# Performance work log

Measured on AMD Instinct MI355X. Metric: run time of the kernel, lower is better.

The kernel has to match this reference:

```python
import jax, jax.numpy as jnp
import numpy as np

MODEL_DIM = 1024
BATCH, SEQ = 4, 2048


def setup_inputs() -> dict:
    key = jax.random.key(0)
    kx, kq, kk, kv = jax.random.split(key, 4)
    s = 1.0 / np.sqrt(MODEL_DIM)
    return {
        "x": jax.random.normal(kx, (BATCH, SEQ, MODEL_DIM), dtype=jnp.float32),
        "Wq": jax.random.normal(kq, (MODEL_DIM, MODEL_DIM), dtype=jnp.float32) * s,
        "Wk": jax.random.normal(kk, (MODEL_DIM, MODEL_DIM), dtype=jnp.float32) * s,
        "Wv": jax.random.normal(kv, (MODEL_DIM, MODEL_DIM), dtype=jnp.float32) * s,
    }


def reference(x, Wq, Wk, Wv):
    # nn.Linear(d, d, bias=False): y = x @ W.T ; W stored [out, in]
    q = jnp.einsum("bsd,ed->bse", x, Wq)
    k = jnp.einsum("bsd,ed->bse", x, Wk)
    v = jnp.einsum("bsd,ed->bse", x, Wv)
    scores = jnp.einsum("bqd,bkd->bqk", q, k) / jnp.sqrt(jnp.float32(MODEL_DIM))
    attn = jax.nn.softmax(scores, axis=-1)
    return jnp.einsum("bqk,bkd->bqd", attn, v)
```

## Files before the change

kernel.cpp:

```cpp
#include <hip/hip_runtime.h>
#include <hip/hip_bf16.h>


typedef short bf16x8_t __attribute__((ext_vector_type(8)));
typedef float f32x4_t __attribute__((ext_vector_type(4)));
typedef unsigned short u16x8_t __attribute__((ext_vector_type(8)));

static __device__ __forceinline__ unsigned short f2bf(float f) {
  __hip_bfloat16 h = __float2bfloat16(f);
  return *reinterpret_cast<unsigned short*>(&h);
}

#define GLOAD_LDS16(gp, lp)                                            \
  __builtin_amdgcn_global_load_lds(                                    \
      (const __attribute__((address_space(1))) void*)(gp),             \
      (__attribute__((address_space(3))) void*)(lp), 16, 0, 0)

__global__ __launch_bounds__(256) void cast_all(
    const float* __restrict__ x, const float* __restrict__ Wq,
    const float* __restrict__ Wk, const float* __restrict__ Wv,
    unsigned short* __restrict__ xb, unsigned short* __restrict__ Wqk,
    unsigned short* __restrict__ Wvb, float* __restrict__ rowsum) {
  int i = blockIdx.x * 256 + threadIdx.x;
  const float* src;
  unsigned short* dst;
  int local;
  if (i < 1048576) {
    src = x; dst = xb; local = i;
  } else {
    int j = i - 1048576;
    int seg = j >> 17;
    if (seg >= 3) {
      int l = j - 393216;
      if (l < 1024) {
        float4 zz = {0.f, 0.f, 0.f, 0.f};
        ((float4*)rowsum)[l * 2] = zz;
        ((float4*)rowsum)[l * 2 + 1] = zz;
      }
      return;
    }
    local = j & 131071;
    src = (seg == 0) ? Wq : ((seg == 1) ? Wk : Wv);
    dst = (seg == 0) ? Wqk : ((seg == 1) ? (Wqk + 1048576) : Wvb);
  }
  float4 a = ((const float4*)src)[local * 2];
  float4 b = ((const float4*)src)[local * 2 + 1];
  u16x8_t o;
  o[0] = f2bf(a.x); o[1] = f2bf(a.y); o[2] = f2bf(a.z); o[3] = f2bf(a.w);
  o[4] = f2bf(b.x); o[5] = f2bf(b.y); o[6] = f2bf(b.z); o[7] = f2bf(b.w);
  ((u16x8_t*)dst)[local] = o;
}

template <int EPI, int BN>
__global__ __launch_bounds__(512, 2) void gemm256p(
    const unsigned short* __restrict__ A, const unsigned short* __restrict__ B,
    void* __restrict__ Cv, float* __restrict__ rowsum, int K, int lda,
    int ldb, int ldc, long long sA, long long sB, long long sC, float alpha,
    int rsz) {
  constexpr int NBG = BN / 64;
  constexpr int NH = NBG / 2;
  constexpr int BL = BN / 128;
  constexpr int BNW = BN / 4;
  constexpr int ASZ = 256 * 64;
  constexpr int BSZ = BN * 64;

  __shared__ unsigned short lds[2][ASZ + BSZ];

  const int gx = gridDim.x, gy = gridDim.y;
  const int nwg = gx * gy * gridDim.z;
  const int orig = (blockIdx.z * gy + blockIdx.y) * gx + blockIdx.x;
  const int swz = (orig & 7) * (nwg >> 3) + (orig >> 3);
  const int bx = swz % gx;
  const int tmp = swz / gx;
  const int by = tmp % gy;
  const int z = tmp / gy;

  const int tid = threadIdx.x;
  const int lane = tid & 63;
  const int w = tid >> 6;
  const int wm = w >> 2, wn = w & 3;
  const int m0 = by * 256, n0 = bx * BN;

  A += (long long)z * sA;
  B += (long long)z * sB;

  int sta_row[2][2], sta_col[2][2], sta_lds[2][2];
#pragma unroll
  for (int mh = 0; mh < 2; ++mh)
#pragma unroll
    for (int i = 0; i < 2; ++i) {
      int j = w * 2 + i;
      int l0 = (j >> 3) * 1024 + mh * 512 + (j & 7) * 64;
      int lf = l0 + lane;
      int R = lf >> 3;
      sta_row[mh][i] = R;
      sta_col[mh][i] = ((lf & 7) ^ (R & 7)) * 8;
      sta_lds[mh][i] = l0 * 8;
    }
  int stb_row[2][BL], stb_col[2][BL], stb_lds[2][BL];
#pragma unroll
  for (int nh = 0; nh < 2; ++nh)
#pragma unroll
    for (int i = 0; i < BL; ++i) {
      int l0;
      if (BL == 2) {
        int j = w * 2 + i;
        l0 = (j >> 2) * 512 + nh * 256 + (j & 3) * 64;
      } else {
        int j = w;
        l0 = (j >> 1) * 256 + nh * 128 + (j & 1) * 64;
      }
      int lf = l0 + lane;
      int R = lf >> 3;
      stb_row[nh][i] = R;
      stb_col[nh][i] = ((lf & 7) ^ (R & 7)) * 8;
      stb_lds[nh][i] = ASZ + l0 * 8;
    }

  const int q = lane >> 4, rl = lane & 15;
  int aoff[8][2], boff[NBG][2];
#pragma unroll
  for (int tt = 0; tt < 8; ++tt)
#pragma unroll
    for (int ks = 0; ks < 2; ++ks) {
      int ra = wm * 128 + tt * 16 + rl;
      aoff[tt][ks] = ra * 64 + (((ks * 4 + q) ^ (ra & 7)) * 8);
    }
#pragma unroll
  for (int u = 0; u < NBG; ++u)
#pragma unroll
    for (int ks = 0; ks < 2; ++ks) {
      int rb = wn * BNW + u * 16 + rl;
      boff[u][ks] = ASZ + rb * 64 + (((ks * 4 + q) ^ (rb & 7)) * 8);
    }

  f32x4_t acc[8][NBG];
#pragma unroll
  for (int i = 0; i < 8; ++i)
#pragma unroll
    for (int j = 0; j < NBG; ++j) acc[i][j] = (f32x4_t){0.f, 0.f, 0.f, 0.f};

#define SA(BUFI, MH, K0)                                                    \
  {                                                                         \
    _Pragma("unroll") for (int i_ = 0; i_ < 2; ++i_)                        \
        GLOAD_LDS16(&A[(long long)(m0 + sta_row[MH][i_]) * lda + (K0) +     \
                       sta_col[MH][i_]],                                    \
                    &lds[BUFI][sta_lds[MH][i_]]);                           \
  }
#define SB(BUFI, NH_, K0)                                                   \
  {                                                                         \
    _Pragma("unroll") for (int i_ = 0; i_ < BL; ++i_)                       \
        GLOAD_LDS16(&B[(long long)(n0 + stb_row[NH_][i_]) * ldb + (K0) +    \
                       stb_col[NH_][i_]],                                   \
                    &lds[BUFI][stb_lds[NH_][i_]]);                          \
  }
#define LDAF(MH)                                                            \
  _Pragma("unroll") for (int i_ = 0; i_ < 4; ++i_)                          \
  _Pragma("unroll") for (int ks_ = 0; ks_ < 2; ++ks_)                       \
      af[i_][ks_] = *(const bf16x8_t*)&L[aoff[(MH)*4 + i_][ks_]];
#define LDBG(NH_)                                                           \
  _Pragma("unroll") for (int j_ = 0; j_ < NH; ++j_)                         \
  _Pragma("unroll") for (int ks_ = 0; ks_ < 2; ++ks_)                       \
      bg[j_][ks_] = *(const bf16x8_t*)&L[boff[(NH_)*NH + j_][ks_]];
#define PH_MFMA(MH, NH_)                                                    \
  __builtin_amdgcn_s_barrier();                                             \
  asm volatile("s_waitcnt lgkmcnt(0)" ::: "memory");                        \
  __builtin_amdgcn_sched_barrier(0);                                        \
  __builtin_amdgcn_s_setprio(1);                                            \
  _Pragma("unroll") for (int ks_ = 0; ks_ < 2; ++ks_)                       \
  _Pragma("unroll") for (int i_ = 0; i_ < 4; ++i_)                          \
  _Pragma("unroll") for (int j_ = 0; j_ < NH; ++j_)                         \
      acc[(MH)*4 + i_][(NH_)*NH + j_] =                                     \
          __builtin_amdgcn_mfma_f32_16x16x32_bf16(                          \
              af[i_][ks_], bg[j_][ks_], acc[(MH)*4 + i_][(NH_)*NH + j_],    \
              0, 0, 0);                                                     \
  __builtin_amdgcn_s_setprio(0);                                            \
  __builtin_amdgcn_sched_barrier(0);                                        \
  __builtin_amdgcn_s_barrier();                                             \
  __builtin_amdgcn_sched_barrier(0);

#define VMC_A()                                                             \
  if constexpr (BL == 2) {                                                  \
    asm volatile("s_waitcnt vmcnt(8)" ::: "memory");                        \
  } else {                                                                  \
    asm volatile("s_waitcnt vmcnt(6)" ::: "memory");                        \
  }                                                                         \
  __builtin_amdgcn_sched_barrier(0);
#define VMC_B()                                                             \
  if constexpr (BL == 2) {                                                  \
    asm volatile("s_waitcnt vmcnt(6)" ::: "memory");                        \
  } else {                                                                  \
    asm volatile("s_waitcnt vmcnt(5)" ::: "memory");                        \
  }                                                                         \
  __builtin_amdgcn_sched_barrier(0);
#define VMC_0()                                                             \
  asm volatile("s_waitcnt vmcnt(0)" ::: "memory");                          \
  __builtin_amdgcn_sched_barrier(0);

#define TILE(T, BU, NX)                                                     \
  {                                                                         \
    const unsigned short* L = lds[BU];                                      \
    const int k1 = ((T) + 1) * 64;                                          \
    const int k2 = ((T) + 2) * 64;                                          \
    const bool p1 = ((T) + 1 < NT), p2 = ((T) + 2 < NT);                    \
    bf16x8_t af[4][2], bg[NH][2];                                           \
                                                           \
    LDAF(0);                                                                \
    LDBG(0);                                                                \
    if (p1) SB(NX, 0, k1);                                                  \
    PH_MFMA(0, 0);                                                          \
                                                           \
    LDBG(1);                                                                \
    if (p1) SA(NX, 1, k1);                                                  \
    if (p2) { VMC_A(); } else { VMC_0(); }                                  \
    PH_MFMA(0, 1);                                                          \
                                                           \
    LDAF(1);                                                                \
    if (p2) SA(BU, 0, k2);                                                  \
    PH_MFMA(1, 1);                                                          \
                                                           \
    LDBG(0);                                                                \
    if (p2) { SB(BU, 1, k2); VMC_B(); } else { VMC_0(); }                   \
    PH_MFMA(1, 0);                                                          \
  }

  const int NT = K >> 6;

  SA(0, 0, 0); SB(0, 0, 0); SB(0, 1, 0); SA(0, 1, 0);
  SA(1, 0, 64); SB(1, 1, 64);
  VMC_B();
  __builtin_amdgcn_s_barrier();
  __builtin_amdgcn_sched_barrier(0);

  for (int t = 0; t < NT; t += 2) {
    TILE(t, 0, 1);
    TILE(t + 1, 1, 0);
  }

  if (EPI == 0) {
    unsigned short* C = (unsigned short*)Cv + (long long)z * sC;
#pragma unroll
    for (int tt = 0; tt < 8; ++tt)
#pragma unroll
      for (int u = 0; u < NBG; ++u)
#pragma unroll
        for (int j = 0; j < 4; ++j) {
          int row = m0 + wm * 128 + tt * 16 + q * 4 + j;
          int col = n0 + wn * BNW + u * 16 + rl;
          C[(long long)row * ldc + col] = f2bf(acc[tt][u][j] * alpha);
        }
  } else if (EPI == 1) {
    unsigned short* C = (unsigned short*)Cv + (long long)z * sC;
#pragma unroll
    for (int tt = 0; tt < 8; ++tt)
#pragma unroll
      for (int j = 0; j < 4; ++j) {
        int row = m0 + wm * 128 + tt * 16 + q * 4 + j;
        float sum = 0.f;
#pragma unroll
        for (int u = 0; u < NBG; ++u) {
          float e = __expf(acc[tt][u][j] * alpha);
          int col = n0 + wn * BNW + u * 16 + rl;
          C[(long long)row * ldc + col] = f2bf(e);
          sum += e;
        }
#pragma unroll
        for (int mk = 1; mk <= 8; mk <<= 1) sum += __shfl_xor(sum, mk);
        if (rl == 0) atomicAdd(&rowsum[z * rsz + row], sum);
      }
  } else {
    float* C = (float*)Cv + (long long)z * sC;
#pragma unroll
    for (int tt = 0; tt < 8; ++tt)
#pragma unroll
      for (int j = 0; j < 4; ++j) {
        int row = m0 + wm * 128 + tt * 16 + q * 4 + j;
        float inv = 1.0f / rowsum[z * rsz + row];
#pragma unroll
        for (int u = 0; u < NBG; ++u) {
          int col = n0 + wn * BNW + u * 16 + rl;
          C[(long long)row * ldc + col] = acc[tt][u][j] * inv;
        }
      }
  }
#undef SA
#undef SB
#undef LDAF
#undef LDBG
#undef PH_MFMA
#undef VMC_A
#undef VMC_B
#undef VMC_0
#undef TILE
}

__global__ __launch_bounds__(256) void gemm_nt128(
    const unsigned short* __restrict__ A, const unsigned short* __restrict__ B,
    unsigned short* __restrict__ C, int K, int lda, int ldb, int ldc) {
  __shared__ unsigned short As[128 * 64];
  __shared__ unsigned short Bs[128 * 64];

  const int gx = gridDim.x, gy = gridDim.y;
  const int nwg = gx * gy;
  const int orig = blockIdx.y * gx + blockIdx.x;
  const int swz = (orig & 7) * (nwg >> 3) + (orig >> 3);
  const int bx = swz % gx;
  const int by = swz / gx;

  const int tid = threadIdx.x;
  const int lane = tid & 63;
  const int w = tid >> 6;
  const int wm = w >> 1, wn = w & 1;
  const int m0 = by * 128;
  const int n0 = bx * 128;

  int srow[4], scol[4];
#pragma unroll
  for (int i = 0; i < 4; ++i) {
    int p = w * 256 + i * 64 + lane;
    int r = p >> 3;
    srow[i] = r;
    scol[i] = ((p & 7) ^ (r & 7)) * 8;
  }

  const int q = lane >> 4, rl = lane & 15;
  int aoff[4][2], boff[4][2];
#pragma unroll
  for (int t = 0; t < 4; ++t)
#pragma unroll
    for (int ks = 0; ks < 2; ++ks) {
      int ra = wm * 64 + t * 16 + rl;
      int ca = ks * 4 + q;
      aoff[t][ks] = ra * 64 + ((ca ^ (ra & 7)) * 8);
      int rb = wn * 64 + t * 16 + rl;
      boff[t][ks] = rb * 64 + ((ca ^ (rb & 7)) * 8);
    }

  f32x4_t acc[4][4];
#pragma unroll
  for (int i = 0; i < 4; ++i)
#pragma unroll
    for (int j = 0; j < 4; ++j) acc[i][j] = (f32x4_t){0.f, 0.f, 0.f, 0.f};

  for (int k0 = 0; k0 < K; k0 += 64) {
    __syncthreads();
#pragma unroll
    for (int i = 0; i < 4; ++i) {
      GLOAD_LDS16(&A[(long long)(m0 + srow[i]) * lda + k0 + scol[i]],
                  &As[(w * 4 + i) * 512]);
      GLOAD_LDS16(&B[(long long)(n0 + srow[i]) * ldb + k0 + scol[i]],
                  &Bs[(w * 4 + i) * 512]);
    }
    __syncthreads();

#pragma unroll
    for (int ks = 0; ks < 2; ++ks) {
      bf16x8_t af[4], bgv[4];
#pragma unroll
      for (int t = 0; t < 4; ++t) af[t] = *(const bf16x8_t*)&As[aoff[t][ks]];
#pragma unroll
      for (int u = 0; u < 4; ++u) bgv[u] = *(const bf16x8_t*)&Bs[boff[u][ks]];
#pragma unroll
      for (int i = 0; i < 4; ++i)
#pragma unroll
        for (int j = 0; j < 4; ++j)
          acc[i][j] = __builtin_amdgcn_mfma_f32_16x16x32_bf16(
              af[i], bgv[j], acc[i][j], 0, 0, 0);
    }
  }

#pragma unroll
  for (int t = 0; t < 4; ++t)
#pragma unroll
    for (int u = 0; u < 4; ++u)
#pragma unroll
      for (int j = 0; j < 4; ++j) {
        int row = m0 + wm * 64 + t * 16 + q * 4 + j;
        int col = n0 + wn * 64 + u * 16 + rl;
        C[(long long)row * ldc + col] = f2bf(acc[t][u][j]);
      }
}

extern "C" void kernel_launch(void* const* d_in, const int* in_sizes, int n_in,
                              void* d_out, int out_size, void* d_ws,
                              size_t ws_size, hipStream_t stream) {
  const float* x = (const float*)d_in[0];
  const float* Wq = (const float*)d_in[1];
  const float* Wk = (const float*)d_in[2];
  const float* Wv = (const float*)d_in[3];
  float* out = (float*)d_out;

  unsigned short* xb = (unsigned short*)d_ws;
  unsigned short* Wqk = xb + 8388608;
  unsigned short* Wvb = Wqk + 2097152;
  unsigned short* Cqk = Wvb + 1048576;
  unsigned short* VTb = Cqk + 16777216;
  unsigned short* Scb = VTb + 8388608;
  float* rowsumf = (float*)(Scb + 16777216);

  const dim3 blk(256);
  const dim3 blk512(512);

  cast_all<<<5636, blk, 0, stream>>>(x, Wq, Wk, Wv, xb, Wqk, Wvb, rowsumf);

  gemm256p<0, 256><<<dim3(8, 32, 1), blk512, 0, stream>>>(
      xb, Wqk, Cqk, nullptr, 1024, 1024, 1024, 2048, 0, 0, 0, 1.0f, 0);

  gemm_nt128<<<dim3(64, 8), blk, 0, stream>>>(Wvb, xb, VTb, 1024, 1024, 1024,
                                              8192);

  gemm256p<1, 256><<<dim3(8, 8, 4), blk512, 0, stream>>>(
      Cqk, Cqk + 1024, Scb, rowsumf, 1024, 2048, 2048, 2048,
      (long long)2048 * 2048, (long long)2048 * 2048,
      (long long)2048 * 2048, 0.03125f, 2048);

  gemm256p<2, 128><<<dim3(8, 8, 4), blk512, 0, stream>>>(
      Scb, VTb, out, rowsumf, 2048, 2048, 8192, 1024,
      (long long)2048 * 2048, 2048, (long long)2048 * 1024, 1.0f, 2048);
}
```

Measured before the change: 160.8 us.

## Specialize GEMM to 256x128 tiles with register-prefetched LDS fragments

The templated 256xBN GEMM becomes a single 256x128 kernel. Its per-tile schedule is restructured so the next tile's A and B fragments are read from LDS into registers while the current MFMAs run, with one barrier per phase instead of two and finer vmcnt waits. The QK projection and score GEMMs switch from 256-wide to 128-wide N tiles, doubling their grid size. The intent is to cut LDS-read latency and barrier stalls and to improve CU occupancy, at the cost of more register pressure and less B-tile reuse per workgroup.

```diff
diff --git a/kernel.cpp b/kernel.cpp
--- a/kernel.cpp
+++ b/kernel.cpp
@@ -51,18 +51,14 @@
   ((u16x8_t*)dst)[local] = o;
 }
 
-template <int EPI, int BN>
-__global__ __launch_bounds__(512, 2) void gemm256p(
+template <int EPI>
+__global__ __launch_bounds__(512, 2) void gemmx(
     const unsigned short* __restrict__ A, const unsigned short* __restrict__ B,
     void* __restrict__ Cv, float* __restrict__ rowsum, int K, int lda,
     int ldb, int ldc, long long sA, long long sB, long long sC, float alpha,
     int rsz) {
-  constexpr int NBG = BN / 64;
-  constexpr int NH = NBG / 2;
-  constexpr int BL = BN / 128;
-  constexpr int BNW = BN / 4;
   constexpr int ASZ = 256 * 64;
-  constexpr int BSZ = BN * 64;
+  constexpr int BSZ = 128 * 64;
 
   __shared__ unsigned short lds[2][ASZ + BSZ];
 
@@ -79,7 +75,7 @@
   const int lane = tid & 63;
   const int w = tid >> 6;
   const int wm = w >> 2, wn = w & 3;
-  const int m0 = by * 256, n0 = bx * BN;
+  const int m0 = by * 256, n0 = bx * 128;
 
   A += (long long)z * sA;
   B += (long long)z * sB;
@@ -97,28 +93,19 @@
       sta_col[mh][i] = ((lf & 7) ^ (R & 7)) * 8;
       sta_lds[mh][i] = l0 * 8;
     }
-  int stb_row[2][BL], stb_col[2][BL], stb_lds[2][BL];
-#pragma unroll
-  for (int nh = 0; nh < 2; ++nh)
-#pragma unroll
-    for (int i = 0; i < BL; ++i) {
-      int l0;
-      if (BL == 2) {
-        int j = w * 2 + i;
-        l0 = (j >> 2) * 512 + nh * 256 + (j & 3) * 64;
-      } else {
-        int j = w;
-        l0 = (j >> 1) * 256 + nh * 128 + (j & 1) * 64;
-      }
-      int lf = l0 + lane;
-      int R = lf >> 3;
-      stb_row[nh][i] = R;
-      stb_col[nh][i] = ((lf & 7) ^ (R & 7)) * 8;
-      stb_lds[nh][i] = ASZ + l0 * 8;
-    }
+  int stb_row[2], stb_col[2], stb_lds[2];
+#pragma unroll
+  for (int nh = 0; nh < 2; ++nh) {
+    int l0 = (w >> 1) * 256 + nh * 128 + (w & 1) * 64;
+    int lf = l0 + lane;
+    int R = lf >> 3;
+    stb_row[nh] = R;
+    stb_col[nh] = ((lf & 7) ^ (R & 7)) * 8;
+    stb_lds[nh] = ASZ + l0 * 8;
+  }
 
   const int q = lane >> 4, rl = lane & 15;
-  int aoff[8][2], boff[NBG][2];
+  int aoff[8][2], boff[2][2];
 #pragma unroll
   for (int tt = 0; tt < 8; ++tt)
 #pragma unroll
@@ -127,18 +114,20 @@
       aoff[tt][ks] = ra * 64 + (((ks * 4 + q) ^ (ra & 7)) * 8);
     }
 #pragma unroll
-  for (int u = 0; u < NBG; ++u)
+  for (int u = 0; u < 2; ++u)
 #pragma unroll
     for (int ks = 0; ks < 2; ++ks) {
-      int rb = wn * BNW + u * 16 + rl;
+      int rb = wn * 32 + u * 16 + rl;
       boff[u][ks] = ASZ + rb * 64 + (((ks * 4 + q) ^ (rb & 7)) * 8);
     }
 
-  f32x4_t acc[8][NBG];
+  f32x4_t acc[8][2];
 #pragma unroll
   for (int i = 0; i < 8; ++i)
 #pragma unroll
-    for (int j = 0; j < NBG; ++j) acc[i][j] = (f32x4_t){0.f, 0.f, 0.f, 0.f};
+    for (int j = 0; j < 2; ++j) acc[i][j] = (f32x4_t){0.f, 0.f, 0.f, 0.f};
+
+  bf16x8_t afA[4][2], afB[4][2], bgY[2], bgX0[2], bgX1[2];
 
 #define SA(BUFI, MH, K0)                                                    \
   {                                                                         \
@@ -148,105 +137,87 @@
                     &lds[BUFI][sta_lds[MH][i_]]);                           \
   }
 #define SB(BUFI, NH_, K0)                                                   \
-  {                                                                         \
-    _Pragma("unroll") for (int i_ = 0; i_ < BL; ++i_)                       \
-        GLOAD_LDS16(&B[(long long)(n0 + stb_row[NH_][i_]) * ldb + (K0) +    \
-                       stb_col[NH_][i_]],                                   \
-                    &lds[BUFI][stb_lds[NH_][i_]]);                          \
-  }
-#define LDAF(MH)                                                            \
+  GLOAD_LDS16(&B[(long long)(n0 + stb_row[NH_]) * ldb + (K0) +              \
+                 stb_col[NH_]],                                             \
+              &lds[BUFI][stb_lds[NH_]]);
+#define RD_AF(DST, L, MH)                                                   \
   _Pragma("unroll") for (int i_ = 0; i_ < 4; ++i_)                          \
   _Pragma("unroll") for (int ks_ = 0; ks_ < 2; ++ks_)                       \
-      af[i_][ks_] = *(const bf16x8_t*)&L[aoff[(MH)*4 + i_][ks_]];
-#define LDBG(NH_)                                                           \
-  _Pragma("unroll") for (int j_ = 0; j_ < NH; ++j_)                         \
+      DST[i_][ks_] = *(const bf16x8_t*)&(L)[aoff[(MH)*4 + i_][ks_]];
+#define RD_BG(DST, L, NH_)                                                  \
   _Pragma("unroll") for (int ks_ = 0; ks_ < 2; ++ks_)                       \
-      bg[j_][ks_] = *(const bf16x8_t*)&L[boff[(NH_)*NH + j_][ks_]];
-#define PH_MFMA(MH, NH_)                                                    \
-  __builtin_amdgcn_s_barrier();                                             \
-  asm volatile("s_waitcnt lgkmcnt(0)" ::: "memory");                        \
+      DST[ks_] = *(const bf16x8_t*)&(L)[boff[NH_][ks_]];
+#define MM(MH, NH_, AF, BG)                                                 \
   __builtin_amdgcn_sched_barrier(0);                                        \
   __builtin_amdgcn_s_setprio(1);                                            \
   _Pragma("unroll") for (int ks_ = 0; ks_ < 2; ++ks_)                       \
   _Pragma("unroll") for (int i_ = 0; i_ < 4; ++i_)                          \
-  _Pragma("unroll") for (int j_ = 0; j_ < NH; ++j_)                         \
-      acc[(MH)*4 + i_][(NH_)*NH + j_] =                                     \
-          __builtin_amdgcn_mfma_f32_16x16x32_bf16(                          \
-              af[i_][ks_], bg[j_][ks_], acc[(MH)*4 + i_][(NH_)*NH + j_],    \
-              0, 0, 0);                                                     \
+      acc[(MH)*4 + i_][NH_] = __builtin_amdgcn_mfma_f32_16x16x32_bf16(      \
+          AF[i_][ks_], BG[ks_], acc[(MH)*4 + i_][NH_], 0, 0, 0);            \
   __builtin_amdgcn_s_setprio(0);                                            \
-  __builtin_amdgcn_sched_barrier(0);                                        \
-  __builtin_amdgcn_s_barrier();                                             \
   __builtin_amdgcn_sched_barrier(0);
 
-#define VMC_A()                                                             \
-  if constexpr (BL == 2) {                                                  \
-    asm volatile("s_waitcnt vmcnt(8)" ::: "memory");                        \
-  } else {                                                                  \
-    asm volatile("s_waitcnt vmcnt(6)" ::: "memory");                        \
-  }                                                                         \
+#define VMC(N)                                                              \
+  asm volatile("s_waitcnt vmcnt(" #N ")" ::: "memory");                     \
   __builtin_amdgcn_sched_barrier(0);
-#define VMC_B()                                                             \
-  if constexpr (BL == 2) {                                                  \
-    asm volatile("s_waitcnt vmcnt(6)" ::: "memory");                        \
-  } else {                                                                  \
-    asm volatile("s_waitcnt vmcnt(5)" ::: "memory");                        \
-  }                                                                         \
-  __builtin_amdgcn_sched_barrier(0);
-#define VMC_0()                                                             \
-  asm volatile("s_waitcnt vmcnt(0)" ::: "memory");                          \
-  __builtin_amdgcn_sched_barrier(0);
-
-#define TILE(T, BU, NX)                                                     \
+
+#define TILE(T, BU, NX, BGXc, BGXn)                                         \
   {                                                                         \
-    const unsigned short* L = lds[BU];                                      \
+    const unsigned short* Lb = lds[BU];                                     \
+    const unsigned short* Ln = lds[NX];                                     \
     const int k1 = ((T) + 1) * 64;                                          \
     const int k2 = ((T) + 2) * 64;                                          \
     const bool p1 = ((T) + 1 < NT), p2 = ((T) + 2 < NT);                    \
-    bf16x8_t af[4][2], bg[NH][2];                                           \
                                                            \
-    LDAF(0);                                                                \
-    LDBG(0);                                                                \
-    if (p1) SB(NX, 0, k1);                                                  \
-    PH_MFMA(0, 0);                                                          \
+    __builtin_amdgcn_s_barrier();                                           \
+    RD_BG(bgY, Lb, 1);                                                      \
+    if (p1) SA(NX, 1, k1);                                                  \
+    MM(0, 0, afA, BGXc);                                                    \
                                                            \
-    LDBG(1);                                                                \
-    if (p1) SA(NX, 1, k1);                                                  \
-    if (p2) { VMC_A(); } else { VMC_0(); }                                  \
-    PH_MFMA(0, 1);                                                          \
+    __builtin_amdgcn_s_barrier();                                           \
+    RD_AF(afB, Lb, 1);                                                      \
+    if (p1) SB(NX, 1, k1);                                                  \
+    MM(0, 1, afA, bgY);                                                     \
+    if (p2) { VMC(4); } else { VMC(0); }                                    \
                                                            \
-    LDAF(1);                                                                \
+    __builtin_amdgcn_s_barrier();                                           \
+    if (p1) RD_AF(afA, Ln, 0);                                              \
     if (p2) SA(BU, 0, k2);                                                  \
-    PH_MFMA(1, 1);                                                          \
+    MM(1, 1, afB, bgY);                                                     \
+    if (p2) { VMC(5); } else { VMC(0); }                                    \
                                                            \
-    LDBG(0);                                                                \
-    if (p2) { SB(BU, 1, k2); VMC_B(); } else { VMC_0(); }                   \
-    PH_MFMA(1, 0);                                                          \
+    __builtin_amdgcn_s_barrier();                                           \
+    if (p1) RD_BG(BGXn, Ln, 0);                                             \
+    if (p2) SB(BU, 0, k2);                                                  \
+    MM(1, 0, afB, BGXc);                                                    \
+    if (p1) { VMC(3); } else { VMC(0); }                                    \
   }
 
   const int NT = K >> 6;
 
-  SA(0, 0, 0); SB(0, 0, 0); SB(0, 1, 0); SA(0, 1, 0);
-  SA(1, 0, 64); SB(1, 1, 64);
-  VMC_B();
+  SA(0, 0, 0); SB(0, 0, 0); SA(0, 1, 0); SB(0, 1, 0);
+  SA(1, 0, 64); SB(1, 0, 64);
+  VMC(3);
   __builtin_amdgcn_s_barrier();
-  __builtin_amdgcn_sched_barrier(0);
+  RD_AF(afA, lds[0], 0);
+  RD_BG(bgX0, lds[0], 0);
 
   for (int t = 0; t < NT; t += 2) {
-    TILE(t, 0, 1);
-    TILE(t + 1, 1, 0);
-  }
+    TILE(t, 0, 1, bgX0, bgX1);
+    TILE(t + 1, 1, 0, bgX1, bgX0);
+  }
+  asm volatile("s_waitcnt vmcnt(0)" ::: "memory");
 
   if (EPI == 0) {
     unsigned short* C = (unsigned short*)Cv + (long long)z * sC;
 #pragma unroll
     for (int tt = 0; tt < 8; ++tt)
 #pragma unroll
-      for (int u = 0; u < NBG; ++u)
+      for (int u = 0; u < 2; ++u)
 #pragma unroll
         for (int j = 0; j < 4; ++j) {
           int row = m0 + wm * 128 + tt * 16 + q * 4 + j;
-          int col = n0 + wn * BNW + u * 16 + rl;
+          int col = n0 + wn * 32 + u * 16 + rl;
           C[(long long)row * ldc + col] = f2bf(acc[tt][u][j] * alpha);
         }
   } else if (EPI == 1) {
@@ -258,9 +229,9 @@
         int row = m0 + wm * 128 + tt * 16 + q * 4 + j;
         float sum = 0.f;
 #pragma unroll
-        for (int u = 0; u < NBG; ++u) {
+        for (int u = 0; u < 2; ++u) {
           float e = __expf(acc[tt][u][j] * alpha);
-          int col = n0 + wn * BNW + u * 16 + rl;
+          int col = n0 + wn * 32 + u * 16 + rl;
           C[(long long)row * ldc + col] = f2bf(e);
           sum += e;
         }
@@ -277,20 +248,18 @@
         int row = m0 + wm * 128 + tt * 16 + q * 4 + j;
         float inv = 1.0f / rowsum[z * rsz + row];
 #pragma unroll
-        for (int u = 0; u < NBG; ++u) {
-          int col = n0 + wn * BNW + u * 16 + rl;
+        for (int u = 0; u < 2; ++u) {
+          int col = n0 + wn * 32 + u * 16 + rl;
           C[(long long)row * ldc + col] = acc[tt][u][j] * inv;
         }
       }
   }
 #undef SA
 #undef SB
-#undef LDAF
-#undef LDBG
-#undef PH_MFMA
-#undef VMC_A
-#undef VMC_B
-#undef VMC_0
+#undef RD_AF
+#undef RD_BG
+#undef MM
+#undef VMC
 #undef TILE
 }
 
@@ -403,18 +372,18 @@
 
   cast_all<<<5636, blk, 0, stream>>>(x, Wq, Wk, Wv, xb, Wqk, Wvb, rowsumf);
 
-  gemm256p<0, 256><<<dim3(8, 32, 1), blk512, 0, stream>>>(
+  gemmx<0><<<dim3(16, 32, 1), blk512, 0, stream>>>(
       xb, Wqk, Cqk, nullptr, 1024, 1024, 1024, 2048, 0, 0, 0, 1.0f, 0);
 
   gemm_nt128<<<dim3(64, 8), blk, 0, stream>>>(Wvb, xb, VTb, 1024, 1024, 1024,
                                               8192);
 
-  gemm256p<1, 256><<<dim3(8, 8, 4), blk512, 0, stream>>>(
+  gemmx<1><<<dim3(16, 8, 4), blk512, 0, stream>>>(
       Cqk, Cqk + 1024, Scb, rowsumf, 1024, 2048, 2048, 2048,
       (long long)2048 * 2048, (long long)2048 * 2048,
       (long long)2048 * 2048, 0.03125f, 2048);
 
-  gemm256p<2, 128><<<dim3(8, 8, 4), blk512, 0, stream>>>(
+  gemmx<2><<<dim3(8, 8, 4), blk512, 0, stream>>>(
       Scb, VTb, out, rowsumf, 2048, 2048, 8192, 1024,
       (long long)2048 * 2048, 2048, (long long)2048 * 1024, 1.0f, 2048);
 }
```

After: 193.3 us. 20.2% more time.
